# Optimization experiments

Measured on AMD Instinct MI355X. Metric: run time of the kernel, lower is better.

Reference implementation:

```python
import jax, jax.numpy as jnp
import numpy as np

B, T, C, H = 2, 2048, 1024, 16
HD = C // H  # 64


def setup_inputs() -> dict:
    key = jax.random.key(0)
    ks = jax.random.split(key, 5)
    x = jax.random.normal(ks[0], (B, T, C), jnp.float32)
    scale = 0.02
    Wq = jax.random.normal(ks[1], (C, C), jnp.float32) * scale
    Wk = jax.random.normal(ks[2], (C, C), jnp.float32) * scale
    Wv = jax.random.normal(ks[3], (C, C), jnp.float32) * scale
    Wo = jax.random.normal(ks[4], (C, C), jnp.float32) * scale
    # RoPE tables: freqs_cis = exp(i * pos * theta_j), theta_j = 10000^(-2j/HD)
    pos = jnp.arange(T, dtype=jnp.float32)
    theta = 10000.0 ** (-jnp.arange(0, HD, 2, dtype=jnp.float32) / HD)  # [HD/2]
    ang = pos[:, None] * theta[None, :]  # [T, HD/2]
    cos = jnp.cos(ang)
    sin = jnp.sin(ang)
    return {"x": x, "Wq": Wq, "Wk": Wk, "Wv": Wv, "Wo": Wo, "cos": cos, "sin": sin}


def _rope(t, cos, sin):
    # t: [B,T,H,HD]; pairs (even, odd) along last dim form complex numbers
    b, s, h, hd = t.shape
    tr = t.reshape(b, s, h, hd // 2, 2)
    t0, t1 = tr[..., 0], tr[..., 1]
    c = cos[None, :, None, :]  # [1,T,1,HD/2]
    sn = sin[None, :, None, :]
    o0 = t0 * c - t1 * sn
    o1 = t0 * sn + t1 * c
    return jnp.stack([o0, o1], axis=-1).reshape(b, s, h, hd)


def reference(x, Wq, Wk, Wv, Wo, cos, sin):
    b, t, c = x.shape
    h, hd = H, c // H
    q = (x @ Wq.T).reshape(b, t, h, hd)
    k = (x @ Wk.T).reshape(b, t, h, hd)
    v = (x @ Wv.T).reshape(b, t, h, hd)
    q = _rope(q, cos, sin)
    k = _rope(k, cos, sin)
    # explicit causal attention with full TxT score matrix (as in source)
    att = jnp.einsum("bthd,bshd->bhts", q, k) / jnp.sqrt(jnp.float32(hd))
    causal = jnp.tril(jnp.ones((t, t), dtype=bool))
    att = jnp.where(causal[None, None, :, :], att, -jnp.inf)
    att = jax.nn.softmax(att, axis=-1)
    out = jnp.einsum("bhts,bshd->bthd", att, v).reshape(b, t, c)
    return out @ Wo.T
```

## Files before the change

### kernel.cpp

```cpp
#include <hip/hip_runtime.h>
#include <cstdint>
#include <cstddef>


typedef __bf16 bf16;
typedef float  f32x4  __attribute__((ext_vector_type(4)));
typedef __bf16 bf16x4 __attribute__((ext_vector_type(4)));
typedef __bf16 bf16x8 __attribute__((ext_vector_type(8)));

constexpr int Bb = 2, Tt = 2048, Cc = 1024, Hh = 16;
constexpr int Mrows = Bb * Tt;
constexpr int NT = Tt / 64;
constexpr int LDS_ = 72;

#define GLOAD_LDS16(gp, lp)                                                      \
    __builtin_amdgcn_global_load_lds(                                            \
        (const __attribute__((address_space(1))) void*)(gp),                     \
        (__attribute__((address_space(3))) void*)(lp), 16, 0, 0)

#define QUAD_T(v0, v1, v2, v3, c2)                                               \
    {                                                                            \
        float e0 = (c2 & 1) ? v0 : v1, e1 = (c2 & 1) ? v2 : v3;                  \
        e0 = __shfl_xor(e0, 1); e1 = __shfl_xor(e1, 1);                          \
        if (c2 & 1) { v0 = e0; v2 = e1; } else { v1 = e0; v3 = e1; }             \
        float f0 = (c2 & 2) ? v0 : v2, f1 = (c2 & 2) ? v1 : v3;                  \
        f0 = __shfl_xor(f0, 2); f1 = __shfl_xor(f1, 2);                          \
        if (c2 & 2) { v0 = f0; v1 = f1; } else { v2 = f0; v3 = f1; }             \
    }

__global__ __launch_bounds__(256) void convert_k(const float* __restrict__ x,
                                                 const float* __restrict__ Wq,
                                                 const float* __restrict__ Wk,
                                                 const float* __restrict__ Wv,
                                                 const float* __restrict__ Wo,
                                                 const float* __restrict__ cosb,
                                                 const float* __restrict__ sinb,
                                                 bf16* __restrict__ xb,
                                                 bf16* __restrict__ Wqkv,
                                                 bf16* __restrict__ Wob,
                                                 float2* __restrict__ cs)
{
    if (blockIdx.x >= 4096) {
        int pi = ((blockIdx.x - 4096) * 256 + threadIdx.x) * 8;
#pragma unroll
        for (int u = 0; u < 8; ++u)
            cs[pi + u] = float2{cosb[pi + u], sinb[pi + u]};
        return;
    }
    uint32_t id = blockIdx.x * 256 + threadIdx.x;
    const float* src; bf16* dst; float sc = 1.0f;
    if (id < 524288u) {
        uint32_t tile = id >> 10, slot = id & 1023;
        uint32_t row = (tile >> 4) * 128 + (slot >> 9) * 64 +
                       ((slot >> 6) & 3) * 16 + (slot & 15);
        uint32_t k = (tile & 15) * 64 + ((slot >> 8) & 1) * 32 + ((slot >> 4) & 3) * 8;
        src = x + (size_t)row * 1024 + k;
        dst = xb + (size_t)id * 8;
    } else if (id < 917504u) {
        uint32_t t2 = id - 524288u;
        uint32_t tile = t2 >> 10, slot = t2 & 1023;
        uint32_t n = (tile >> 4) * 128 + (slot >> 9) * 64 +
                     ((slot >> 6) & 3) * 16 + (slot & 15);
        uint32_t k = (tile & 15) * 64 + ((slot >> 8) & 1) * 32 + ((slot >> 4) & 3) * 8;
        if (n < 1024)      { src = Wq + (size_t)n * 1024 + k;
                             sc = 0.125f * 1.44269504088896f; }
        else if (n < 2048)   src = Wk + (size_t)(n - 1024) * 1024 + k;
        else                 src = Wv + (size_t)(n - 2048) * 1024 + k;
        dst = Wqkv + (size_t)t2 * 8;
    } else {
        uint32_t t3 = id - 917504u;
        uint32_t tile = t3 >> 9, slot = t3 & 511;
        uint32_t n = (tile >> 4) * 64 + (slot >> 8) * 32 +
                     ((slot >> 6) & 1) * 16 + (slot & 15);
        uint32_t k = (tile & 15) * 64 + ((slot >> 7) & 1) * 32 + ((slot >> 4) & 3) * 8;
        src = Wo + (size_t)n * 1024 + k;
        dst = Wob + (size_t)t3 * 8;
    }
    float4 v0 = *(const float4*)(src);
    float4 v1 = *(const float4*)(src + 4);
    bf16x8 t;
    t[0] = (bf16)(v0.x*sc); t[1] = (bf16)(v0.y*sc); t[2] = (bf16)(v0.z*sc); t[3] = (bf16)(v0.w*sc);
    t[4] = (bf16)(v1.x*sc); t[5] = (bf16)(v1.y*sc); t[6] = (bf16)(v1.z*sc); t[7] = (bf16)(v1.w*sc);
    *(bf16x8*)dst = t;
}

__global__ __launch_bounds__(256) void gemm_qkv(const bf16* __restrict__ A,
                                                const bf16* __restrict__ W,
                                                bf16* __restrict__ QK,
                                                bf16* __restrict__ Vt,
                                                const float2* __restrict__ cs)
{
    __shared__ bf16 As[8192];
    __shared__ bf16 Ws[8192];
    const int tid  = threadIdx.x;
    const int lane = tid & 63, wave = tid >> 6;
    const int rhw = wave >> 1, chw = wave & 1;
    const int wr = rhw * 64, wc = chw * 64;
    const int l16 = lane & 15, lq = lane >> 4;
    const int row0 = blockIdx.x * 128, col0 = blockIdx.y * 128;

    f32x4 acc[4][4];
#pragma unroll
    for (int i = 0; i < 4; ++i)
#pragma unroll
        for (int j = 0; j < 4; ++j) acc[i][j] = f32x4{0.f, 0.f, 0.f, 0.f};

    const bf16* At = A + (size_t)blockIdx.x * 16 * 8192;
    const bf16* Wt = W + (size_t)blockIdx.y * 16 * 8192;

    for (int kb = 0; kb < 16; ++kb) {
        const bf16* at = At + kb * 8192;
        const bf16* wt = Wt + kb * 8192;
#pragma unroll
        for (int rnd = 0; rnd < 4; ++rnd) {
            const int seg = rnd * 4 + wave;
            GLOAD_LDS16(at + seg * 512 + lane * 8, &As[seg * 512]);
            GLOAD_LDS16(wt + seg * 512 + lane * 8, &Ws[seg * 512]);
        }
        __syncthreads();
#pragma unroll
        for (int ks = 0; ks < 2; ++ks) {
            bf16x8 af[4], bfr[4];
#pragma unroll
            for (int i = 0; i < 4; ++i)
                af[i] = *(const bf16x8*)(&As[(rhw * 512 + ks * 256 + i * 64 + lq * 16 + l16) * 8]);
#pragma unroll
            for (int j = 0; j < 4; ++j)
                bfr[j] = *(const bf16x8*)(&Ws[(chw * 512 + ks * 256 + j * 64 + lq * 16 + l16) * 8]);
#pragma unroll
            for (int i = 0; i < 4; ++i)
#pragma unroll
                for (int j = 0; j < 4; ++j)
                    acc[i][j] = __builtin_amdgcn_mfma_f32_16x16x32_bf16(
                        af[i], bfr[j], acc[i][j], 0, 0, 0);
        }
        __syncthreads();
    }

    const int c2 = l16 & 3, g4 = (l16 >> 2) * 4;
    if (blockIdx.y < 16) {
#pragma unroll
        for (int i = 0; i < 4; ++i)
#pragma unroll
            for (int j = 0; j < 4; ++j) {
                float v0 = acc[i][j][0], v1 = acc[i][j][1];
                float v2 = acc[i][j][2], v3 = acc[i][j][3];
                QUAD_T(v0, v1, v2, v3, c2);
                const int row = row0 + wr + i * 16 + lq * 4 + c2;
                const int t   = row & (Tt - 1);
                const int colb = wc + j * 16 + g4;
                const int p0   = (colb & 63) >> 1;
                float4 cp = *(const float4*)(&cs[t * 32 + p0]);
                bf16x4 pk;
                pk[0] = (bf16)(v0 * cp.x - v1 * cp.y);
                pk[1] = (bf16)(v0 * cp.y + v1 * cp.x);
                pk[2] = (bf16)(v2 * cp.z - v3 * cp.w);
                pk[3] = (bf16)(v2 * cp.w + v3 * cp.z);
                *(bf16x4*)(&QK[(size_t)row * 2048 + col0 + colb]) = pk;
            }
    } else {
#pragma unroll
        for (int i = 0; i < 4; ++i)
#pragma unroll
            for (int j = 0; j < 4; ++j) {
                const int dfull = col0 - 2048 + wc + j * 16 + l16;
                const int h = dfull >> 6, d = dfull & 63;
                const int row = row0 + wr + i * 16 + lq * 4;
                const int b = row >> 11, t = row & (Tt - 1);
                bf16x4 pk;
                pk[0] = (bf16)acc[i][j][0]; pk[1] = (bf16)acc[i][j][1];
                pk[2] = (bf16)acc[i][j][2]; pk[3] = (bf16)acc[i][j][3];
                *(bf16x4*)(&Vt[((size_t)(b * 16 + h) * 64 + d) * (size_t)Tt + t]) = pk;
            }
    }
}

__global__ __launch_bounds__(256) void gemm_o(const bf16* __restrict__ A,
                                              const bf16* __restrict__ W,
                                              float* __restrict__ Out)
{
    __shared__ bf16 As[8192];
    __shared__ bf16 Ws[4096];
    const int tid  = threadIdx.x;
    const int lane = tid & 63, wave = tid >> 6;
    const int rhw = wave >> 1, chw = wave & 1;
    const int wr = rhw * 64, wc = chw * 32;
    const int l16 = lane & 15, lq = lane >> 4;
    const int row0 = blockIdx.x * 128, col0 = blockIdx.y * 64;

    f32x4 acc[4][2];
#pragma unroll
    for (int i = 0; i < 4; ++i)
#pragma unroll
        for (int j = 0; j < 2; ++j) acc[i][j] = f32x4{0.f, 0.f, 0.f, 0.f};

    const bf16* At = A + (size_t)blockIdx.x * 16 * 8192;
    const bf16* Wt = W + (size_t)blockIdx.y * 16 * 4096;

    for (int kb = 0; kb < 16; ++kb) {
        const bf16* at = At + kb * 8192;
        const bf16* wt = Wt + kb * 4096;
#pragma unroll
        for (int rnd = 0; rnd < 4; ++rnd) {
            const int seg = rnd * 4 + wave;
            GLOAD_LDS16(at + seg * 512 + lane * 8, &As[seg * 512]);
        }
#pragma unroll
        for (int rnd = 0; rnd < 2; ++rnd) {
            const int seg = rnd * 4 + wave;
            GLOAD_LDS16(wt + seg * 512 + lane * 8, &Ws[seg * 512]);
        }
        __syncthreads();
#pragma unroll
        for (int ks = 0; ks < 2; ++ks) {
            bf16x8 af[4], bfr[2];
#pragma unroll
            for (int i = 0; i < 4; ++i)
                af[i] = *(const bf16x8*)(&As[(rhw * 512 + ks * 256 + i * 64 + lq * 16 + l16) * 8]);
#pragma unroll
            for (int j = 0; j < 2; ++j)
                bfr[j] = *(const bf16x8*)(&Ws[(chw * 256 + ks * 128 + j * 64 + lq * 16 + l16) * 8]);
#pragma unroll
            for (int i = 0; i < 4; ++i)
#pragma unroll
                for (int j = 0; j < 2; ++j)
                    acc[i][j] = __builtin_amdgcn_mfma_f32_16x16x32_bf16(
                        af[i], bfr[j], acc[i][j], 0, 0, 0);
        }
        __syncthreads();
    }
    const int c2 = l16 & 3, g4 = (l16 >> 2) * 4;
#pragma unroll
    for (int i = 0; i < 4; ++i)
#pragma unroll
        for (int j = 0; j < 2; ++j) {
            float v0 = acc[i][j][0], v1 = acc[i][j][1];
            float v2 = acc[i][j][2], v3 = acc[i][j][3];
            QUAD_T(v0, v1, v2, v3, c2);
            const int row = row0 + wr + i * 16 + lq * 4 + c2;
            const int col = col0 + wc + j * 16 + g4;
            *(float4*)(&Out[(size_t)row * Cc + col]) = float4{v0, v1, v2, v3};
        }
}

__global__ __launch_bounds__(256, 4) void attn_k(const bf16* __restrict__ QK,
                                                 const bf16* __restrict__ Vt,
                                                 bf16* __restrict__ O)
{
    __shared__ bf16 Ks[2][64 * LDS_];
    __shared__ bf16 Vs[2][64 * LDS_];
    const int tid = threadIdx.x;
    const int wv = tid >> 6, lane = tid & 63;
    const int l16 = lane & 15, lq = lane >> 4;
    const int id = blockIdx.y * gridDim.x + blockIdx.x;
    const int bh = (id & 7) * 4 + ((id >> 3) & 3);
    const int sIdx = (id >> 5) & 7, rnd4 = id >> 8;
    const int qt = (rnd4 == 0) ? 31 - sIdx : (rnd4 == 1) ? 16 + sIdx
                 : (rnd4 == 2) ? 15 - sIdx : sIdx;
    const int b = bh >> 4, h = bh & 15;
    const int kr = tid >> 2, c0 = (tid & 3) * 16;
    const int pr = 32 * (kr >> 5) + 16 * ((kr >> 2) & 1) + 4 * ((kr >> 3) & 3) + (kr & 3);

    const bf16* kcol = QK + 1024 + (size_t)(b * Tt + kr) * 2048 + h * 64 + c0;
    const bf16* vcol = Vt + ((size_t)bh * 64 + kr) * Tt + c0;

    const int qglob = qt * 64 + wv * 16 + l16;
    const bf16* qp = QK + (size_t)(b * Tt + qglob) * 2048 + h * 64;
    bf16x8 qf0 = *(const bf16x8*)(qp + lq * 8);
    bf16x8 qf1 = *(const bf16x8*)(qp + 32 + lq * 8);

    bf16x8 onef;
#pragma unroll
    for (int r = 0; r < 8; ++r) onef[r] = (bf16)1.0f;

    uint4 pk0 = *(const uint4*)(kcol);
    uint4 pk1 = *(const uint4*)(kcol + 8);
    uint4 pv0 = *(const uint4*)(vcol);
    uint4 pv1 = *(const uint4*)(vcol + 8);
    *(uint4*)(&Ks[0][pr * LDS_ + c0])     = pk0;
    *(uint4*)(&Ks[0][pr * LDS_ + c0 + 8]) = pk1;
    *(uint4*)(&Vs[0][kr * LDS_ + c0])     = pv0;
    *(uint4*)(&Vs[0][kr * LDS_ + c0 + 8]) = pv1;
    __syncthreads();

    f32x4 accl = f32x4{0.f, 0.f, 0.f, 0.f};
    f32x4 o[4];
#pragma unroll
    for (int dt = 0; dt < 4; ++dt) o[dt] = f32x4{0.f, 0.f, 0.f, 0.f};

    for (int t = 0; t <= qt; ++t) {
        const int cur = t & 1;
        if (t < qt) {
            const bf16* kn = kcol + (size_t)(t + 1) * 64 * 2048;
            const bf16* vn = vcol + (t + 1) * 64;
            pk0 = *(const uint4*)(kn);
            pk1 = *(const uint4*)(kn + 8);
            pv0 = *(const uint4*)(vn);
            pv1 = *(const uint4*)(vn + 8);
        }

        f32x4 s[4];
#pragma unroll
        for (int mt = 0; mt < 4; ++mt) s[mt] = f32x4{0.f, 0.f, 0.f, 0.f};
#pragma unroll
        for (int mt = 0; mt < 4; ++mt) {
            bf16x8 a0 = *(const bf16x8*)(&Ks[cur][(mt * 16 + l16) * LDS_ + lq * 8]);
            s[mt] = __builtin_amdgcn_mfma_f32_16x16x32_bf16(a0, qf0, s[mt], 0, 0, 0);
        }
#pragma unroll
        for (int mt = 0; mt < 4; ++mt) {
            bf16x8 a1 = *(const bf16x8*)(&Ks[cur][(mt * 16 + l16) * LDS_ + 32 + lq * 8]);
            s[mt] = __builtin_amdgcn_mfma_f32_16x16x32_bf16(a1, qf1, s[mt], 0, 0, 0);
        }
        if (t == qt) {
            const int qloc = wv * 16 + l16;
#pragma unroll
            for (int mt = 0; mt < 4; ++mt)
#pragma unroll
                for (int r = 0; r < 4; ++r) {
                    int keyl = (mt >> 1) * 32 + lq * 8 + (mt & 1) * 4 + r;
                    if (keyl > qloc) s[mt][r] = -1e30f;
                }
        }
        bf16x8 pb0, pb1;
#pragma unroll
        for (int mt = 0; mt < 4; ++mt)
#pragma unroll
            for (int r = 0; r < 4; ++r)
                s[mt][r] = exp2f(s[mt][r]);
#pragma unroll
        for (int r = 0; r < 4; ++r) {
            pb0[r]     = (bf16)s[0][r];
            pb0[4 + r] = (bf16)s[1][r];
            pb1[r]     = (bf16)s[2][r];
            pb1[4 + r] = (bf16)s[3][r];
        }
        accl = __builtin_amdgcn_mfma_f32_16x16x32_bf16(onef, pb0, accl, 0, 0, 0);
        accl = __builtin_amdgcn_mfma_f32_16x16x32_bf16(onef, pb1, accl, 0, 0, 0);
#pragma unroll
        for (int dt = 0; dt < 4; ++dt) {
            bf16x8 v0 = *(const bf16x8*)(&Vs[cur][(dt * 16 + l16) * LDS_ + lq * 8]);
            o[dt] = __builtin_amdgcn_mfma_f32_16x16x32_bf16(v0, pb0, o[dt], 0, 0, 0);
        }
#pragma unroll
        for (int dt = 0; dt < 4; ++dt) {
            bf16x8 v1 = *(const bf16x8*)(&Vs[cur][(dt * 16 + l16) * LDS_ + 32 + lq * 8]);
            o[dt] = __builtin_amdgcn_mfma_f32_16x16x32_bf16(v1, pb1, o[dt], 0, 0, 0);
        }
        if (t < qt) {
            *(uint4*)(&Ks[cur ^ 1][pr * LDS_ + c0])     = pk0;
            *(uint4*)(&Ks[cur ^ 1][pr * LDS_ + c0 + 8]) = pk1;
            *(uint4*)(&Vs[cur ^ 1][kr * LDS_ + c0])     = pv0;
            *(uint4*)(&Vs[cur ^ 1][kr * LDS_ + c0 + 8]) = pv1;
        }
        __syncthreads();
    }
    float inv = 1.f / accl[0];
    bf16* obase = O + ((size_t)(b * 16 + (qt >> 1)) * 16 + h) * 8192;
    const int rh = qt & 1;
#pragma unroll
    for (int dt = 0; dt < 4; ++dt) {
        bf16x4 pk;
#pragma unroll
        for (int r = 0; r < 4; ++r) pk[r] = (bf16)(o[dt][r] * inv);
        const int slot = rh * 512 + (dt >> 1) * 256 + wv * 64 +
                         ((dt & 1) * 2 + (lq >> 1)) * 16 + l16;
        *(bf16x4*)(obase + slot * 8 + (lq & 1) * 4) = pk;
    }
}

extern "C" void kernel_launch(void* const* d_in, const int* in_sizes, int n_in,
                              void* d_out, int out_size, void* d_ws, size_t ws_size,
                              hipStream_t stream)
{
    const float* x    = (const float*)d_in[0];
    const float* Wq   = (const float*)d_in[1];
    const float* Wk   = (const float*)d_in[2];
    const float* Wv   = (const float*)d_in[3];
    const float* Wo   = (const float*)d_in[4];
    const float* cosb = (const float*)d_in[5];
    const float* sinb = (const float*)d_in[6];

    constexpr size_t M1 = 1024 * 1024;
    bf16* base = (bf16*)d_ws;
    bf16*   xb   = base;
    bf16*   QK   = base + 4 * M1;
    bf16*   VtG  = base + 12 * M1;
    bf16*   Wqkv = base + 16 * M1;
    bf16*   Wob  = base + 19 * M1;
    float2* csT  = (float2*)(base + 20 * M1);
    bf16*   Ow   = xb;

    convert_k<<<4096 + 32, 256, 0, stream>>>(x, Wq, Wk, Wv, Wo, cosb, sinb,
                                             xb, Wqkv, Wob, csT);

    gemm_qkv<<<dim3(Mrows / 128, 3072 / 128), 256, 0, stream>>>(
        xb, Wqkv, QK, VtG, csT);

    attn_k<<<dim3(NT, Bb * Hh), 256, 0, stream>>>(QK, VtG, Ow);

    gemm_o<<<dim3(Mrows / 128, Cc / 64), 256, 0, stream>>>(Ow, Wob, (float*)d_out);
}
```

Baseline: 169.2 us.

## Rewrite attention with 32x32 MFMA tiles and 128-row query blocks

New measurement: 183.3 us. +8.4%, slower.

```diff
diff --git a/kernel.cpp b/kernel.cpp
--- a/kernel.cpp
+++ b/kernel.cpp
@@ -5,6 +5,7 @@
 
 typedef __bf16 bf16;
 typedef float  f32x4  __attribute__((ext_vector_type(4)));
+typedef float  f32x16 __attribute__((ext_vector_type(16)));
 typedef __bf16 bf16x4 __attribute__((ext_vector_type(4)));
 typedef __bf16 bf16x8 __attribute__((ext_vector_type(8)));
 
@@ -27,6 +28,13 @@
         f0 = __shfl_xor(f0, 2); f1 = __shfl_xor(f1, 2);                          \
         if (c2 & 2) { v0 = f0; v1 = f1; } else { v2 = f0; v3 = f1; }             \
     }
+
+__device__ inline unsigned pkb(float a, float b)
+{
+    unsigned r;
+    asm("v_cvt_pk_bf16_f32 %0, %1, %2" : "=v"(r) : "v"(a), "v"(b));
+    return r;
+}
 
 __global__ __launch_bounds__(256) void convert_k(const float* __restrict__ x,
                                                  const float* __restrict__ Wq,
@@ -243,7 +251,7 @@
         }
 }
 
-__global__ __launch_bounds__(256, 4) void attn_k(const bf16* __restrict__ QK,
+__global__ __launch_bounds__(256, 2) void attn_k(const bf16* __restrict__ QK,
                                                  const bf16* __restrict__ Vt,
                                                  bf16* __restrict__ O)
 {
@@ -251,46 +259,43 @@
     __shared__ bf16 Vs[2][64 * LDS_];
     const int tid = threadIdx.x;
     const int wv = tid >> 6, lane = tid & 63;
-    const int l16 = lane & 15, lq = lane >> 4;
+    const int l31 = lane & 31, hf = lane >> 5;
     const int id = blockIdx.y * gridDim.x + blockIdx.x;
     const int bh = (id & 7) * 4 + ((id >> 3) & 3);
-    const int sIdx = (id >> 5) & 7, rnd4 = id >> 8;
-    const int qt = (rnd4 == 0) ? 31 - sIdx : (rnd4 == 1) ? 16 + sIdx
-                 : (rnd4 == 2) ? 15 - sIdx : sIdx;
+    const int sIdx = (id >> 5) & 7, rnd = id >> 8;
+    const int gq = rnd ? (15 - sIdx) : sIdx;
     const int b = bh >> 4, h = bh & 15;
+    const int nsteps = 2 * gq + 2;
     const int kr = tid >> 2, c0 = (tid & 3) * 16;
-    const int pr = 32 * (kr >> 5) + 16 * ((kr >> 2) & 1) + 4 * ((kr >> 3) & 3) + (kr & 3);
 
     const bf16* kcol = QK + 1024 + (size_t)(b * Tt + kr) * 2048 + h * 64 + c0;
     const bf16* vcol = Vt + ((size_t)bh * 64 + kr) * Tt + c0;
 
-    const int qglob = qt * 64 + wv * 16 + l16;
-    const bf16* qp = QK + (size_t)(b * Tt + qglob) * 2048 + h * 64;
-    bf16x8 qf0 = *(const bf16x8*)(qp + lq * 8);
-    bf16x8 qf1 = *(const bf16x8*)(qp + 32 + lq * 8);
-
-    bf16x8 onef;
-#pragma unroll
-    for (int r = 0; r < 8; ++r) onef[r] = (bf16)1.0f;
+    const int qglob = gq * 128 + wv * 32 + l31;
+    const bf16* qp = QK + (size_t)(b * Tt + qglob) * 2048 + h * 64 + hf * 8;
+    bf16x8 qf[4];
+#pragma unroll
+    for (int kc = 0; kc < 4; ++kc)
+        qf[kc] = *(const bf16x8*)(qp + kc * 16);
 
     uint4 pk0 = *(const uint4*)(kcol);
     uint4 pk1 = *(const uint4*)(kcol + 8);
     uint4 pv0 = *(const uint4*)(vcol);
     uint4 pv1 = *(const uint4*)(vcol + 8);
-    *(uint4*)(&Ks[0][pr * LDS_ + c0])     = pk0;
-    *(uint4*)(&Ks[0][pr * LDS_ + c0 + 8]) = pk1;
+    *(uint4*)(&Ks[0][kr * LDS_ + c0])     = pk0;
+    *(uint4*)(&Ks[0][kr * LDS_ + c0 + 8]) = pk1;
     *(uint4*)(&Vs[0][kr * LDS_ + c0])     = pv0;
     *(uint4*)(&Vs[0][kr * LDS_ + c0 + 8]) = pv1;
     __syncthreads();
 
-    f32x4 accl = f32x4{0.f, 0.f, 0.f, 0.f};
-    f32x4 o[4];
-#pragma unroll
-    for (int dt = 0; dt < 4; ++dt) o[dt] = f32x4{0.f, 0.f, 0.f, 0.f};
-
-    for (int t = 0; t <= qt; ++t) {
+    float la = 0.f, lb = 0.f, lc = 0.f, ld = 0.f;
+    f32x16 o0, o1;
+#pragma unroll
+    for (int r = 0; r < 16; ++r) { o0[r] = 0.f; o1[r] = 0.f; }
+
+    for (int t = 0; t < nsteps; ++t) {
         const int cur = t & 1;
-        if (t < qt) {
+        if (t + 1 < nsteps) {
             const bf16* kn = kcol + (size_t)(t + 1) * 64 * 2048;
             const bf16* vn = vcol + (t + 1) * 64;
             pk0 = *(const uint4*)(kn);
@@ -299,73 +304,86 @@
             pv1 = *(const uint4*)(vn + 8);
         }
 
-        f32x4 s[4];
-#pragma unroll
-        for (int mt = 0; mt < 4; ++mt) s[mt] = f32x4{0.f, 0.f, 0.f, 0.f};
-#pragma unroll
-        for (int mt = 0; mt < 4; ++mt) {
-            bf16x8 a0 = *(const bf16x8*)(&Ks[cur][(mt * 16 + l16) * LDS_ + lq * 8]);
-            s[mt] = __builtin_amdgcn_mfma_f32_16x16x32_bf16(a0, qf0, s[mt], 0, 0, 0);
-        }
-#pragma unroll
-        for (int mt = 0; mt < 4; ++mt) {
-            bf16x8 a1 = *(const bf16x8*)(&Ks[cur][(mt * 16 + l16) * LDS_ + 32 + lq * 8]);
-            s[mt] = __builtin_amdgcn_mfma_f32_16x16x32_bf16(a1, qf1, s[mt], 0, 0, 0);
-        }
-        if (t == qt) {
-            const int qloc = wv * 16 + l16;
-#pragma unroll
-            for (int mt = 0; mt < 4; ++mt)
-#pragma unroll
-                for (int r = 0; r < 4; ++r) {
-                    int keyl = (mt >> 1) * 32 + lq * 8 + (mt & 1) * 4 + r;
-                    if (keyl > qloc) s[mt][r] = -1e30f;
-                }
-        }
-        bf16x8 pb0, pb1;
-#pragma unroll
-        for (int mt = 0; mt < 4; ++mt)
-#pragma unroll
-            for (int r = 0; r < 4; ++r)
-                s[mt][r] = exp2f(s[mt][r]);
-#pragma unroll
-        for (int r = 0; r < 4; ++r) {
-            pb0[r]     = (bf16)s[0][r];
-            pb0[4 + r] = (bf16)s[1][r];
-            pb1[r]     = (bf16)s[2][r];
-            pb1[4 + r] = (bf16)s[3][r];
-        }
-        accl = __builtin_amdgcn_mfma_f32_16x16x32_bf16(onef, pb0, accl, 0, 0, 0);
-        accl = __builtin_amdgcn_mfma_f32_16x16x32_bf16(onef, pb1, accl, 0, 0, 0);
-#pragma unroll
-        for (int dt = 0; dt < 4; ++dt) {
-            bf16x8 v0 = *(const bf16x8*)(&Vs[cur][(dt * 16 + l16) * LDS_ + lq * 8]);
-            o[dt] = __builtin_amdgcn_mfma_f32_16x16x32_bf16(v0, pb0, o[dt], 0, 0, 0);
-        }
-#pragma unroll
-        for (int dt = 0; dt < 4; ++dt) {
-            bf16x8 v1 = *(const bf16x8*)(&Vs[cur][(dt * 16 + l16) * LDS_ + 32 + lq * 8]);
-            o[dt] = __builtin_amdgcn_mfma_f32_16x16x32_bf16(v1, pb1, o[dt], 0, 0, 0);
-        }
-        if (t < qt) {
-            *(uint4*)(&Ks[cur ^ 1][pr * LDS_ + c0])     = pk0;
-            *(uint4*)(&Ks[cur ^ 1][pr * LDS_ + c0 + 8]) = pk1;
+        f32x16 s0, s1;
+#pragma unroll
+        for (int r = 0; r < 16; ++r) { s0[r] = 0.f; s1[r] = 0.f; }
+#pragma unroll
+        for (int kc = 0; kc < 4; ++kc) {
+            bf16x8 a = *(const bf16x8*)(&Ks[cur][l31 * LDS_ + kc * 16 + hf * 8]);
+            s0 = __builtin_amdgcn_mfma_f32_32x32x16_bf16(a, qf[kc], s0, 0, 0, 0);
+        }
+#pragma unroll
+        for (int kc = 0; kc < 4; ++kc) {
+            bf16x8 a = *(const bf16x8*)(&Ks[cur][(32 + l31) * LDS_ + kc * 16 + hf * 8]);
+            s1 = __builtin_amdgcn_mfma_f32_32x32x16_bf16(a, qf[kc], s1, 0, 0, 0);
+        }
+        if (t >= 2 * gq) {
+            const int kbase = t * 64 + 4 * hf;
+#pragma unroll
+            for (int r = 0; r < 16; ++r) {
+                const int key0 = kbase + (r & 3) + 8 * (r >> 2);
+                if (key0 > qglob)      s0[r] = -1e30f;
+                if (key0 + 32 > qglob) s1[r] = -1e30f;
+            }
+        }
+#pragma unroll
+        for (int r = 0; r < 16; ++r) {
+            s0[r] = exp2f(s0[r]);
+            s1[r] = exp2f(s1[r]);
+            if (r & 1) { lb += s0[r]; ld += s1[r]; }
+            else       { la += s0[r]; lc += s1[r]; }
+        }
+        bf16x8 pb[4];
+#pragma unroll
+        for (int c = 0; c < 4; ++c) {
+            const f32x16& sv = (c < 2) ? s0 : s1;
+            const int rb = (c & 1) * 8;
+            unsigned X = pkb(sv[rb + 0], sv[rb + 1]);
+            unsigned Y = pkb(sv[rb + 2], sv[rb + 3]);
+            unsigned Z = pkb(sv[rb + 4], sv[rb + 5]);
+            unsigned W = pkb(sv[rb + 6], sv[rb + 7]);
+            asm("v_permlane32_swap_b32 %0, %1" : "+v"(X), "+v"(Z));
+            asm("v_permlane32_swap_b32 %0, %1" : "+v"(Y), "+v"(W));
+            union { unsigned u[4]; bf16x8 h; } tmp;
+            tmp.u[0] = X; tmp.u[1] = Y; tmp.u[2] = Z; tmp.u[3] = W;
+            pb[c] = tmp.h;
+        }
+#pragma unroll
+        for (int c = 0; c < 4; ++c) {
+            bf16x8 v = *(const bf16x8*)(&Vs[cur][l31 * LDS_ + c * 16 + hf * 8]);
+            o0 = __builtin_amdgcn_mfma_f32_32x32x16_bf16(v, pb[c], o0, 0, 0, 0);
+        }
+#pragma unroll
+        for (int c = 0; c < 4; ++c) {
+            bf16x8 v = *(const bf16x8*)(&Vs[cur][(32 + l31) * LDS_ + c * 16 + hf * 8]);
+            o1 = __builtin_amdgcn_mfma_f32_32x32x16_bf16(v, pb[c], o1, 0, 0, 0);
+        }
+        if (t + 1 < nsteps) {
+            *(uint4*)(&Ks[cur ^ 1][kr * LDS_ + c0])     = pk0;
+            *(uint4*)(&Ks[cur ^ 1][kr * LDS_ + c0 + 8]) = pk1;
             *(uint4*)(&Vs[cur ^ 1][kr * LDS_ + c0])     = pv0;
             *(uint4*)(&Vs[cur ^ 1][kr * LDS_ + c0 + 8]) = pv1;
         }
         __syncthreads();
     }
-    float inv = 1.f / accl[0];
-    bf16* obase = O + ((size_t)(b * 16 + (qt >> 1)) * 16 + h) * 8192;
-    const int rh = qt & 1;
-#pragma unroll
-    for (int dt = 0; dt < 4; ++dt) {
-        bf16x4 pk;
-#pragma unroll
-        for (int r = 0; r < 4; ++r) pk[r] = (bf16)(o[dt][r] * inv);
-        const int slot = rh * 512 + (dt >> 1) * 256 + wv * 64 +
-                         ((dt & 1) * 2 + (lq >> 1)) * 16 + l16;
-        *(bf16x4*)(obase + slot * 8 + (lq & 1) * 4) = pk;
+    float lsum = (la + lb) + (lc + ld);
+    lsum += __shfl_xor(lsum, 32);
+    float inv = 1.f / lsum;
+
+    bf16* obase = O + ((size_t)(16 * b + gq) * 16 + h) * 8192;
+    const int slot_row = (lane & 15) | (((2 * wv + ((lane >> 4) & 1)) & 3) << 6) |
+                         (((wv >> 1) & 1) << 9);
+#pragma unroll
+    for (int dt = 0; dt < 2; ++dt) {
+        const f32x16& ov = dt ? o1 : o0;
+#pragma unroll
+        for (int g = 0; g < 4; ++g) {
+            bf16x4 pk;
+#pragma unroll
+            for (int r = 0; r < 4; ++r) pk[r] = (bf16)(ov[4 * g + r] * inv);
+            const int slot = slot_row | (g << 4) | (dt << 8);
+            *(bf16x4*)(obase + slot * 8 + 4 * hf) = pk;
+        }
     }
 }
 
@@ -397,7 +415,7 @@
     gemm_qkv<<<dim3(Mrows / 128, 3072 / 128), 256, 0, stream>>>(
         xb, Wqkv, QK, VtG, csT);
 
-    attn_k<<<dim3(NT, Bb * Hh), 256, 0, stream>>>(QK, VtG, Ow);
+    attn_k<<<dim3(32, 16), 256, 0, stream>>>(QK, VtG, Ow);
 
     gemm_o<<<dim3(Mrows / 128, Cc / 64), 256, 0, stream>>>(Ow, Wob, (float*)d_out);
 }
```
